# Optimization experiments

Hardware: AMD Instinct MI355X
Metric: run time of the kernel (lower is better)

The kernel has to match this reference:

```python
import jax, jax.numpy as jnp
import numpy as np
import math

B, C, H, W = 4, 256, 64, 64
E = 96  # embed_dim
SOFTMAX_SCALE = 10.0
RESIDUAL_SCALE_INIT = 0.1


def conv1x1(w, x):
    # w: [out_c, in_c], x: [b, in_c, h, w] -> [b, out_c, h, w]
    return jnp.einsum('oc,bchw->bohw', w, x)


def setup_inputs() -> dict:
    key = jax.random.key(0)
    ks = jax.random.split(key, 12)
    s = 0.02
    return {
        'x': jax.random.normal(ks[0], (B, C, H, W), jnp.float32),
        'mask': jax.random.uniform(ks[1], (B, 1, H, W), jnp.float32),
        'ln_gamma': jnp.ones((C,), jnp.float32),
        'ln_beta': jnp.zeros((C,), jnp.float32),
        'wq': jax.random.normal(ks[2], (E, C), jnp.float32) * s,
        'wk': jax.random.normal(ks[3], (E, C), jnp.float32) * s,
        'wv': jax.random.normal(ks[4], (C, C), jnp.float32) * s,
        'w_out': jax.random.normal(ks[5], (C, C), jnp.float32) * s,
        'w_qm': jax.random.normal(ks[6], (E, 1), jnp.float32) * s,
        'wd1': jax.random.normal(ks[7], (C, 2 * C), jnp.float32) * s,
        'wd2': jax.random.normal(ks[8], (C, C), jnp.float32) * s,
        'wg': jax.random.normal(ks[9], (C, C + 1), jnp.float32) * s,
        'residual_scale': jnp.asarray(RESIDUAL_SCALE_INIT, jnp.float32),
    }


def reference(x, mask, ln_gamma, ln_beta, wq, wk, wv, w_out, w_qm, wd1, wd2, wg,
              residual_scale):
    b, c, h, w = x.shape
    n = h * w

    # ChannelLayerNorm: LayerNorm over channel dim
    mu = jnp.mean(x, axis=1, keepdims=True)
    var = jnp.mean((x - mu) ** 2, axis=1, keepdims=True)
    x_norm = (x - mu) / jnp.sqrt(var + 1e-5)
    x_norm = x_norm * ln_gamma[None, :, None, None] + ln_beta[None, :, None, None]

    # Q/K/V projections (1x1 convs), flatten to [b, n, d]
    q = conv1x1(wq, x_norm) + conv1x1(w_qm, mask)
    q = q.reshape(b, E, n).transpose(0, 2, 1)        # [b, n, E]
    k = conv1x1(wk, x_norm).reshape(b, E, n).transpose(0, 2, 1)  # [b, n, E]
    v = conv1x1(wv, x).reshape(b, c, n).transpose(0, 2, 1)       # [b, n, C]

    # cosine normalization (F.normalize with eps=1e-12)
    q = q / jnp.clip(jnp.linalg.norm(q, axis=-1, keepdims=True), 1e-12)
    k = k / jnp.clip(jnp.linalg.norm(k, axis=-1, keepdims=True), 1e-12)

    scale = SOFTMAX_SCALE / math.sqrt(E)
    attn = jnp.einsum('bqe,bke->bqk', q, k) * scale  # [b, n, n]

    # keys with mask >= 0.5 are invalid -> bias -10000
    invalid_keys = (mask.reshape(b, 1, n) >= 0.5)    # [b, 1, n]
    attn = jnp.where(invalid_keys, jnp.float32(-10000.0), attn)
    attn = jax.nn.softmax(attn, axis=-1)

    attended = jnp.einsum('bqk,bkc->bqc', attn, v)   # [b, n, C]
    attended = attended.transpose(0, 2, 1).reshape(b, c, h, w)
    attended = conv1x1(w_out, attended)

    # delta correction branch
    corr_in = jnp.concatenate([attended - x, x_norm * mask], axis=1)  # [b, 2C, h, w]
    hidden = jax.nn.gelu(conv1x1(wd1, corr_in), approximate=False)
    corrective = conv1x1(wd2, hidden)

    # MaskConditionedGate (assumed): sigmoid(1x1 conv over [corrective, mask])
    gate_in = jnp.concatenate([corrective, mask], axis=1)  # [b, C+1, h, w]
    gate = jax.nn.sigmoid(conv1x1(wg, gate_in)) * mask

    delta = jnp.tanh(residual_scale) * gate * corrective
    return x + delta
```

## Files before the change

### kernel.cpp

```cpp
#include <hip/hip_runtime.h>
#include <hip/hip_bf16.h>
#include <math.h>

#define BB 4
#define CC 256
#define NN 4096
#define EE 96
#define NTOT (BB*NN)

typedef __attribute__((ext_vector_type(8))) short bf16x8;
typedef __attribute__((ext_vector_type(4))) float f32x4;

__device__ __forceinline__ short f2bf(float x) {
    __hip_bfloat16 h = __float2bfloat16(x);
    return *reinterpret_cast<short*>(&h);
}
__device__ __forceinline__ float bf2f(short s) {
    unsigned int u = ((unsigned int)(unsigned short)s) << 16;
    float f;
    __builtin_memcpy(&f, &u, 4);
    return f;
}
__device__ __forceinline__ float gelu_exact(float v) {
    return 0.5f * v * (1.0f + erff(v * 0.70710678118654752f));
}
__device__ __forceinline__ void gld16(void* lds, const void* g) {
    __builtin_amdgcn_global_load_lds(
        (const __attribute__((address_space(1))) unsigned int*)g,
        (__attribute__((address_space(3))) unsigned int*)lds, 16, 0, 0);
}

#define OFF_WQ  0
#define OFF_WK  24576
#define OFF_WV  49152
#define OFF_WO  114688
#define OFF_WD1 180224
#define OFF_WD2 311296
#define OFF_WG  376832
#define OFF_WGL 442368
#define W16_TOTAL 442624

__global__ void wconv_kernel(const float* __restrict__ wq, const float* __restrict__ wk,
                             const float* __restrict__ wv, const float* __restrict__ wo,
                             const float* __restrict__ wd1, const float* __restrict__ wd2,
                             const float* __restrict__ wg, short* __restrict__ W16) {
    int i = blockIdx.x * 256 + threadIdx.x;
    if (i >= W16_TOTAL) return;
    float v;
    if      (i < OFF_WK)  v = wq[i];
    else if (i < OFF_WV)  v = wk[i - OFF_WK];
    else if (i < OFF_WO)  v = wv[i - OFF_WV];
    else if (i < OFF_WD1) v = wo[i - OFF_WO];
    else if (i < OFF_WD2) v = wd1[i - OFF_WD1];
    else if (i < OFF_WG)  v = wd2[i - OFF_WD2];
    else if (i < OFF_WGL) { int l = i - OFF_WG; v = wg[(l >> 8) * 257 + (l & 255)]; }
    else                  v = wg[(i - OFF_WGL) * 257 + 256];
    W16[i] = f2bf(v);
}

__global__ __launch_bounds__(256) void lnproj_kernel(
    const float* __restrict__ x, const float* __restrict__ gamma,
    const float* __restrict__ beta, const short* __restrict__ W16,
    const float* __restrict__ mask, const float* __restrict__ w_qm,
    short* __restrict__ Xt16, short* __restrict__ Xn16,
    short* __restrict__ Q16, short* __restrict__ K16,
    short* __restrict__ V16t)
{
    __shared__ char ldsbuf[17408];
    float* tile = (float*)ldsbuf;
    short* Vt   = (short*)ldsbuf;
    __shared__ short Xn_lds[16 * 264];
    __shared__ short Xt_lds[16 * 264];
    __shared__ float psum[16][16], psq[16][16];
    __shared__ float mu_s[16], rs_s[16];
    __shared__ float gs[256], bs[256];

    const int tid = threadIdx.x;
    const int w = tid >> 6, lane = tid & 63, ln = lane & 15, quad = lane >> 4;
    const int b  = blockIdx.x >> 8;
    const int p0 = (blockIdx.x & 255) * 16;
    const int m0 = blockIdx.x * 16;
    const float* xb = x + (size_t)b * CC * NN;

    gs[tid] = gamma[tid];
    bs[tid] = beta[tid];
    #pragma unroll
    for (int i = 0; i < 4; ++i) {
        int idx = tid + i * 256;
        int c = idx >> 2, p4 = (idx & 3) * 4;
        float4 v = *(const float4*)&xb[(size_t)c * NN + p0 + p4];
        tile[c * 17 + p4]     = v.x;
        tile[c * 17 + p4 + 1] = v.y;
        tile[c * 17 + p4 + 2] = v.z;
        tile[c * 17 + p4 + 3] = v.w;
    }
    __syncthreads();
    {
        int col = tid & 15, part = tid >> 4;
        float s = 0.f, sq = 0.f;
        for (int r = part * 16; r < part * 16 + 16; ++r) {
            float v = tile[r * 17 + col];
            s += v; sq += v * v;
        }
        psum[part][col] = s; psq[part][col] = sq;
    }
    __syncthreads();
    if (tid < 16) {
        float S = 0.f, SQ = 0.f;
        #pragma unroll
        for (int j = 0; j < 16; ++j) { S += psum[j][tid]; SQ += psq[j][tid]; }
        float mu = S / 256.0f;
        float var = SQ / 256.0f - mu * mu;
        mu_s[tid] = mu;
        rs_s[tid] = rsqrtf(var + 1e-5f);
    }
    __syncthreads();
    #pragma unroll
    for (int i = 0; i < 2; ++i) {
        int idx = tid + i * 256;
        int p = idx >> 5, c8 = (idx & 31) * 8;
        float mu = mu_s[p], rcp = rs_s[p];
        bf16x8 xt, xn;
        #pragma unroll
        for (int j = 0; j < 8; ++j) {
            float v = tile[(c8 + j) * 17 + p];
            float n = (v - mu) * rcp * gs[c8 + j] + bs[c8 + j];
            xt[j] = f2bf(v); xn[j] = f2bf(n);
        }
        size_t o = (size_t)(m0 + p) * CC + c8;
        *(bf16x8*)&Xt16[o] = xt;
        *(bf16x8*)&Xn16[o] = xn;
        *(bf16x8*)&Xt_lds[p * 264 + c8] = xt;
        *(bf16x8*)&Xn_lds[p * 264 + c8] = xn;
    }
    asm volatile("s_waitcnt lgkmcnt(0)" ::: "memory");
    __builtin_amdgcn_s_barrier();
    __builtin_amdgcn_sched_barrier(0);

    if (w < 2) {
        const bool isQ = (w == 0);
        const int woff = isQ ? OFF_WQ : OFF_WK;

        f32x4 acc[6];
        #pragma unroll
        for (int i = 0; i < 6; ++i) acc[i] = (f32x4){0.f, 0.f, 0.f, 0.f};

        #pragma unroll
        for (int kt = 0; kt < 8; ++kt) {
            bf16x8 af = *(const bf16x8*)&Xn_lds[ln * 264 + kt * 32 + quad * 8];
            #pragma unroll
            for (int nt = 0; nt < 6; ++nt) {
                bf16x8 bf = *(const bf16x8*)&W16[woff + (size_t)(nt * 16 + ln) * 256 + kt * 32 + quad * 8];
                acc[nt] = __builtin_amdgcn_mfma_f32_16x16x32_bf16(af, bf, acc[nt], 0, 0, 0);
            }
        }

        short* outp = isQ ? Q16 : K16;
        #pragma unroll
        for (int r = 0; r < 4; ++r) {
            int row = m0 + quad * 4 + r;
            float mrow = isQ ? mask[row] : 0.f;
            float vals[6];
            float ss = 0.f;
            #pragma unroll
            for (int nt = 0; nt < 6; ++nt) {
                float v = acc[nt][r];
                if (isQ) v += mrow * w_qm[nt * 16 + ln];
                vals[nt] = v;
                ss += v * v;
            }
            ss += __shfl_xor(ss, 1, 64); ss += __shfl_xor(ss, 2, 64);
            ss += __shfl_xor(ss, 4, 64); ss += __shfl_xor(ss, 8, 64);
            float sc = 1.0f / fmaxf(sqrtf(ss), 1e-12f);
            #pragma unroll
            for (int nt = 0; nt < 6; ++nt)
                outp[(size_t)row * EE + nt * 16 + ln] = f2bf(vals[nt] * sc);
        }
    } else {
        const int wn = w - 2;

        f32x4 acc[8];
        #pragma unroll
        for (int i = 0; i < 8; ++i) acc[i] = (f32x4){0.f, 0.f, 0.f, 0.f};

        #pragma unroll
        for (int kt = 0; kt < 8; ++kt) {
            bf16x8 af = *(const bf16x8*)&Xt_lds[ln * 264 + kt * 32 + quad * 8];
            #pragma unroll
            for (int nt = 0; nt < 8; ++nt) {
                int col = wn * 128 + nt * 16 + ln;
                bf16x8 bf = *(const bf16x8*)&W16[OFF_WV + (size_t)col * 256 + kt * 32 + quad * 8];
                acc[nt] = __builtin_amdgcn_mfma_f32_16x16x32_bf16(af, bf, acc[nt], 0, 0, 0);
            }
        }
        #pragma unroll
        for (int nt = 0; nt < 8; ++nt) {
            int ch = wn * 128 + nt * 16 + ln;
            #pragma unroll
            for (int r = 0; r < 4; ++r)
                Vt[ch * 24 + quad * 4 + r] = f2bf(acc[nt][r]);
        }
    }
    asm volatile("s_waitcnt lgkmcnt(0)" ::: "memory");
    __builtin_amdgcn_s_barrier();
    __builtin_amdgcn_sched_barrier(0);

    #pragma unroll
    for (int i = 0; i < 2; ++i) {
        int idx = tid + i * 256;
        int ch = idx >> 1, p8 = (idx & 1) * 8;
        *(bf16x8*)&V16t[((size_t)b * CC + ch) * NN + p0 + p8] =
            *(const bf16x8*)&Vt[ch * 24 + p8];
    }
}

__global__ __launch_bounds__(256, 4) void attn_kernel(
    const short* __restrict__ Q16, const short* __restrict__ K16,
    const short* __restrict__ V16t, const float* __restrict__ mask,
    short* __restrict__ Opart, float* __restrict__ Lpart)
{
    __shared__ short Ks[2][3072];
    __shared__ short Ps[2][2560];

    const int tid = threadIdx.x;
    const int w = tid >> 6, lane = tid & 63, ln = lane & 15, quad = lane >> 4;
    const int bidx = blockIdx.x;
    const int kg = bidx >> 8;
    const int qg = bidx & 255;
    const int b  = (qg & 7) >> 1;
    const int qt = ((qg >> 3) << 1) | (qg & 1);
    const int q0 = qt * 64;
    const size_t bN = (size_t)b * NN;
    const size_t bCC = (size_t)b * CC;
    const int kbase = kg * 1024;
    const float C1 = 1.02062072615966f;
    const int wbase = w * 64;

    #define STAGEK(buf, kk)                                                         \
        do {                                                                        \
            gld16(&Ks[buf][wbase * 8],                                              \
                  &K16[(bN + (kk) + (tid & 31)) * EE + (tid >> 5) * 8]);            \
            if (w < 2)                                                              \
                gld16(&Ks[buf][(256 + wbase) * 8],                                  \
                      &K16[(bN + (kk) + (tid & 31)) * EE + (8 + (tid >> 5)) * 8]);  \
        } while (0)

    bf16x8 qf[3];
    #pragma unroll
    for (int e = 0; e < 3; ++e)
        qf[e] = *(const bf16x8*)&Q16[(bN + q0 + w * 16 + ln) * EE + e * 32 + quad * 8];

    f32x4 acc[4][4];
    #pragma unroll
    for (int mt = 0; mt < 4; ++mt)
        #pragma unroll
        for (int nt = 0; nt < 4; ++nt) acc[mt][nt] = (f32x4){0.f, 0.f, 0.f, 0.f};
    float lsum[4] = {0.f, 0.f, 0.f, 0.f};

    STAGEK(0, kbase);
    STAGEK(1, kbase + 32);
    __syncthreads();

    for (int it = 0; it < 32; ++it) {
        const int k0 = kbase + it * 32;
        const int cur = it & 1;

        bf16x8 vf[4];
        #pragma unroll
        for (int nt = 0; nt < 4; ++nt)
            vf[nt] = *(const bf16x8*)&V16t[(bCC + wbase + nt * 16 + ln) * NN + k0 + quad * 8];
        const float mk0 = mask[bN + k0 + ln];
        const float mk1 = mask[bN + k0 + 16 + ln];

        f32x4 s0 = (f32x4){0.f,0.f,0.f,0.f}, s1 = s0;
        __builtin_amdgcn_s_setprio(1);
        #pragma unroll
        for (int e = 0; e < 3; ++e) {
            bf16x8 kf0 = *(const bf16x8*)&Ks[cur][((e * 4 + quad) * 32 + ln) * 8];
            bf16x8 kf1 = *(const bf16x8*)&Ks[cur][((e * 4 + quad) * 32 + 16 + ln) * 8];
            s0 = __builtin_amdgcn_mfma_f32_16x16x32_bf16(qf[e], kf0, s0, 0, 0, 0);
            s1 = __builtin_amdgcn_mfma_f32_16x16x32_bf16(qf[e], kf1, s1, 0, 0, 0);
        }
        __builtin_amdgcn_s_setprio(0);
        const bool z0 = mk0 >= 0.5f;
        const bool z1 = mk1 >= 0.5f;
        #pragma unroll
        for (int r = 0; r < 4; ++r) {
            float p0 = z0 ? 0.f : __expf(fmaf(s0[r], C1, -C1));
            float p1 = z1 ? 0.f : __expf(fmaf(s1[r], C1, -C1));
            lsum[r] += p0 + p1;
            Ps[cur][(w * 16 + quad * 4 + r) * 40 + ln]      = f2bf(p0);
            Ps[cur][(w * 16 + quad * 4 + r) * 40 + 16 + ln] = f2bf(p1);
        }
        asm volatile("s_waitcnt vmcnt(0) lgkmcnt(0)" ::: "memory");
        __builtin_amdgcn_s_barrier();
        __builtin_amdgcn_sched_barrier(0);

        if (it + 2 < 32) STAGEK(cur, k0 + 64);

        __builtin_amdgcn_s_setprio(1);
        #pragma unroll
        for (int mt = 0; mt < 4; ++mt) {
            bf16x8 pf = *(const bf16x8*)&Ps[cur][(mt * 16 + ln) * 40 + quad * 8];
            #pragma unroll
            for (int nt = 0; nt < 4; ++nt)
                acc[mt][nt] = __builtin_amdgcn_mfma_f32_16x16x32_bf16(pf, vf[nt], acc[mt][nt], 0, 0, 0);
        }
        __builtin_amdgcn_s_setprio(0);
    }
    #undef STAGEK

    #pragma unroll
    for (int r = 0; r < 4; ++r) {
        float l = lsum[r];
        l += __shfl_xor(l, 1, 64); l += __shfl_xor(l, 2, 64);
        l += __shfl_xor(l, 4, 64); l += __shfl_xor(l, 8, 64);
        if (ln == 0)
            Lpart[(size_t)kg * NTOT + bN + q0 + w * 16 + quad * 4 + r] = l;
    }
    #pragma unroll
    for (int mt = 0; mt < 4; ++mt)
        #pragma unroll
        for (int nt = 0; nt < 4; ++nt)
            #pragma unroll
            for (int r = 0; r < 4; ++r)
                Opart[((size_t)kg * NTOT + bN + q0 + mt * 16 + quad * 4 + r) * 256
                      + wbase + nt * 16 + ln] = f2bf(acc[mt][nt][r]);
}

__global__ __launch_bounds__(256, 4) void epi_kernel(
    const short* __restrict__ Opart, const float* __restrict__ Lpart,
    const short* __restrict__ W16, const short* __restrict__ Xt16,
    const short* __restrict__ Xn16, const float* __restrict__ mask,
    const float* __restrict__ rs, const float* __restrict__ x,
    float* __restrict__ out)
{
    __shared__ char lds[37696];
    short* Olds  = (short*)lds;
    short* Clds  = (short*)lds;
    short* Dlds  = (short*)(lds + 8448);
    short* Hlds  = (short*)(lds + 25344);
    short* tileB = (short*)(lds + 25344);
    float* lsh   = (float*)(lds + 37632);

    const int tid = threadIdx.x;
    const int w = tid >> 6, lane = tid & 63, ln = lane & 15, quad = lane >> 4;
    const int m0 = blockIdx.x * 16;
    const int b = m0 >> 12, p0l = m0 & 4095;

    if (tid < 16) {
        int g = m0 + tid;
        lsh[tid] = 1.0f / (Lpart[g] + Lpart[NTOT + g] + Lpart[2 * NTOT + g] + Lpart[3 * NTOT + g]);
    }
    __syncthreads();

    #pragma unroll
    for (int i = 0; i < 2; ++i) {
        int idx = tid + i * 256;
        int q = idx >> 5, ch8 = (idx & 31) * 8;
        size_t base = (size_t)(m0 + q) * 256 + ch8;
        bf16x8 a0 = *(const bf16x8*)&Opart[base];
        bf16x8 a1 = *(const bf16x8*)&Opart[(size_t)NTOT * 256 + base];
        bf16x8 a2 = *(const bf16x8*)&Opart[(size_t)2 * NTOT * 256 + base];
        bf16x8 a3 = *(const bf16x8*)&Opart[(size_t)3 * NTOT * 256 + base];
        float linv = lsh[q];
        bf16x8 o;
        #pragma unroll
        for (int e = 0; e < 8; ++e)
            o[e] = f2bf((bf2f(a0[e]) + bf2f(a1[e]) + bf2f(a2[e]) + bf2f(a3[e])) * linv);
        *(bf16x8*)&Olds[q * 264 + ch8] = o;
        bf16x8 xn = *(const bf16x8*)&Xn16[base];
        float mq = mask[m0 + q];
        bf16x8 xm;
        #pragma unroll
        for (int e = 0; e < 8; ++e) xm[e] = f2bf(bf2f(xn[e]) * mq);
        *(bf16x8*)&Dlds[q * 528 + 256 + ch8] = xm;
    }
    __syncthreads();

    {
        f32x4 acc[4];
        #pragma unroll
        for (int i = 0; i < 4; ++i) acc[i] = (f32x4){0.f, 0.f, 0.f, 0.f};
        #pragma unroll
        for (int kt = 0; kt < 8; ++kt) {
            bf16x8 af = *(const bf16x8*)&Olds[ln * 264 + kt * 32 + quad * 8];
            #pragma unroll
            for (int nt = 0; nt < 4; ++nt) {
                int col = w * 64 + nt * 16 + ln;
                bf16x8 bf = *(const bf16x8*)&W16[OFF_WO + (size_t)col * 256 + kt * 32 + quad * 8];
                acc[nt] = __builtin_amdgcn_mfma_f32_16x16x32_bf16(af, bf, acc[nt], 0, 0, 0);
            }
        }
        #pragma unroll
        for (int nt = 0; nt < 4; ++nt) {
            int col = w * 64 + nt * 16 + ln;
            #pragma unroll
            for (int r = 0; r < 4; ++r) {
                int row = quad * 4 + r;
                float v = acc[nt][r] - bf2f(Xt16[(size_t)(m0 + row) * 256 + col]);
                Dlds[row * 528 + col] = f2bf(v);
            }
        }
    }
    __syncthreads();

    {
        f32x4 acc[4];
        #pragma unroll
        for (int i = 0; i < 4; ++i) acc[i] = (f32x4){0.f, 0.f, 0.f, 0.f};
        #pragma unroll
        for (int kt = 0; kt < 16; ++kt) {
            bf16x8 af = *(const bf16x8*)&Dlds[ln * 528 + kt * 32 + quad * 8];
            #pragma unroll
            for (int nt = 0; nt < 4; ++nt) {
                int col = w * 64 + nt * 16 + ln;
                bf16x8 bf = *(const bf16x8*)&W16[OFF_WD1 + (size_t)col * 512 + kt * 32 + quad * 8];
                acc[nt] = __builtin_amdgcn_mfma_f32_16x16x32_bf16(af, bf, acc[nt], 0, 0, 0);
            }
        }
        #pragma unroll
        for (int nt = 0; nt < 4; ++nt) {
            int col = w * 64 + nt * 16 + ln;
            #pragma unroll
            for (int r = 0; r < 4; ++r) {
                int row = quad * 4 + r;
                Hlds[row * 264 + col] = f2bf(gelu_exact(acc[nt][r]));
            }
        }
    }
    __syncthreads();

    {
        f32x4 acc[4];
        #pragma unroll
        for (int i = 0; i < 4; ++i) acc[i] = (f32x4){0.f, 0.f, 0.f, 0.f};
        #pragma unroll
        for (int kt = 0; kt < 8; ++kt) {
            bf16x8 af = *(const bf16x8*)&Hlds[ln * 264 + kt * 32 + quad * 8];
            #pragma unroll
            for (int nt = 0; nt < 4; ++nt) {
                int col = w * 64 + nt * 16 + ln;
                bf16x8 bf = *(const bf16x8*)&W16[OFF_WD2 + (size_t)col * 256 + kt * 32 + quad * 8];
                acc[nt] = __builtin_amdgcn_mfma_f32_16x16x32_bf16(af, bf, acc[nt], 0, 0, 0);
            }
        }
        #pragma unroll
        for (int nt = 0; nt < 4; ++nt) {
            int col = w * 64 + nt * 16 + ln;
            #pragma unroll
            for (int r = 0; r < 4; ++r) {
                int row = quad * 4 + r;
                Clds[row * 264 + col] = f2bf(acc[nt][r]);
            }
        }
    }
    __syncthreads();

    {
        f32x4 acc[4];
        #pragma unroll
        for (int i = 0; i < 4; ++i) acc[i] = (f32x4){0.f, 0.f, 0.f, 0.f};
        #pragma unroll
        for (int kt = 0; kt < 8; ++kt) {
            bf16x8 af = *(const bf16x8*)&Clds[ln * 264 + kt * 32 + quad * 8];
            #pragma unroll
            for (int nt = 0; nt < 4; ++nt) {
                int col = w * 64 + nt * 16 + ln;
                bf16x8 bf = *(const bf16x8*)&W16[OFF_WG + (size_t)col * 256 + kt * 32 + quad * 8];
                acc[nt] = __builtin_amdgcn_mfma_f32_16x16x32_bf16(af, bf, acc[nt], 0, 0, 0);
            }
        }
        float trs = tanhf(rs[0]);
        #pragma unroll
        for (int nt = 0; nt < 4; ++nt) {
            int col = w * 64 + nt * 16 + ln;
            float wgl = bf2f(W16[OFF_WGL + col]);
            #pragma unroll
            for (int r = 0; r < 4; ++r) {
                int row = quad * 4 + r;
                float mrow = mask[m0 + row];
                float logit = acc[nt][r] + mrow * wgl;
                float gate = mrow / (1.0f + __expf(-logit));
                float corr = bf2f(Clds[row * 264 + col]);
                tileB[col * 24 + row] = f2bf(trs * gate * corr);
            }
        }
    }
    __syncthreads();

    #pragma unroll
    for (int i = 0; i < 2; ++i) {
        int idx = tid + i * 256;
        int ch = idx >> 1, p8 = (idx & 1) * 8;
        bf16x8 d = *(const bf16x8*)&tileB[ch * 24 + p8];
        size_t o = ((size_t)b * CC + ch) * NN + p0l + p8;
        float4 x0 = *(const float4*)&x[o];
        float4 x1 = *(const float4*)&x[o + 4];
        float4 o0, o1;
        o0.x = x0.x + bf2f(d[0]); o0.y = x0.y + bf2f(d[1]);
        o0.z = x0.z + bf2f(d[2]); o0.w = x0.w + bf2f(d[3]);
        o1.x = x1.x + bf2f(d[4]); o1.y = x1.y + bf2f(d[5]);
        o1.z = x1.z + bf2f(d[6]); o1.w = x1.w + bf2f(d[7]);
        *(float4*)&out[o] = o0;
        *(float4*)&out[o + 4] = o1;
    }
}

extern "C" void kernel_launch(void* const* d_in, const int* in_sizes, int n_in,
                              void* d_out, int out_size, void* d_ws, size_t ws_size,
                              hipStream_t stream) {
    const float* x     = (const float*)d_in[0];
    const float* mask  = (const float*)d_in[1];
    const float* gamma = (const float*)d_in[2];
    const float* beta  = (const float*)d_in[3];
    const float* wq    = (const float*)d_in[4];
    const float* wk    = (const float*)d_in[5];
    const float* wv    = (const float*)d_in[6];
    const float* w_out = (const float*)d_in[7];
    const float* w_qm  = (const float*)d_in[8];
    const float* wd1   = (const float*)d_in[9];
    const float* wd2   = (const float*)d_in[10];
    const float* wg    = (const float*)d_in[11];
    const float* rs    = (const float*)d_in[12];
    float* out = (float*)d_out;

    const size_t NC = (size_t)NTOT * CC;
    const size_t NE = (size_t)NTOT * EE;
    short* Xn16  = (short*)d_ws;
    short* Xt16  = Xn16 + NC;
    short* Q16   = Xt16 + NC;
    short* K16   = Q16 + NE;
    short* V16t  = K16 + NE;
    short* W16   = V16t + NC;
    short* Opart = W16 + W16_TOTAL;
    float* Lpart = (float*)(Opart + 4 * NC);

    wconv_kernel<<<(W16_TOTAL + 255) / 256, 256, 0, stream>>>(wq, wk, wv, w_out,
                                                              wd1, wd2, wg, W16);
    lnproj_kernel<<<1024, 256, 0, stream>>>(x, gamma, beta, W16, mask, w_qm,
                                            Xt16, Xn16, Q16, K16, V16t);
    attn_kernel<<<1024, 256, 0, stream>>>(Q16, K16, V16t, mask, Opart, Lpart);
    epi_kernel<<<1024, 256, 0, stream>>>(Opart, Lpart, W16, Xt16, Xn16, mask,
                                         rs, x, out);
}
```

Measured before the change: 289.1 us.

## Hoist epilogue global loads, use exp2 softmax, bit-trick bf16 rounding, vectorize weight convert

Several independent micro-optimizations. A hand-written round-to-nearest-even bf16 conversion replaces the library call, and the softmax exponent is folded into exp2f with a prescaled constant. The weight-conversion kernel now handles four elements per thread with a vector store. The epilogue issues its Opart, Xn16, mask and Xt16 global loads before the first barrier so their latency overlaps the Lpart reduction, at the cost of more registers.

Result: no change. 293.9 us (+1.7%).

```diff
diff --git a/kernel.cpp b/kernel.cpp
--- a/kernel.cpp
+++ b/kernel.cpp
@@ -12,8 +12,10 @@
 typedef __attribute__((ext_vector_type(4))) float f32x4;
 
 __device__ __forceinline__ short f2bf(float x) {
-    __hip_bfloat16 h = __float2bfloat16(x);
-    return *reinterpret_cast<short*>(&h);
+    unsigned int u;
+    __builtin_memcpy(&u, &x, 4);
+    u += 0x7FFFu + ((u >> 16) & 1u);
+    return (short)(u >> 16);
 }
 __device__ __forceinline__ float bf2f(short s) {
     unsigned int u = ((unsigned int)(unsigned short)s) << 16;
@@ -44,18 +46,24 @@
                              const float* __restrict__ wv, const float* __restrict__ wo,
                              const float* __restrict__ wd1, const float* __restrict__ wd2,
                              const float* __restrict__ wg, short* __restrict__ W16) {
-    int i = blockIdx.x * 256 + threadIdx.x;
-    if (i >= W16_TOTAL) return;
-    float v;
-    if      (i < OFF_WK)  v = wq[i];
-    else if (i < OFF_WV)  v = wk[i - OFF_WK];
-    else if (i < OFF_WO)  v = wv[i - OFF_WV];
-    else if (i < OFF_WD1) v = wo[i - OFF_WO];
-    else if (i < OFF_WD2) v = wd1[i - OFF_WD1];
-    else if (i < OFF_WG)  v = wd2[i - OFF_WD2];
-    else if (i < OFF_WGL) { int l = i - OFF_WG; v = wg[(l >> 8) * 257 + (l & 255)]; }
-    else                  v = wg[(i - OFF_WGL) * 257 + 256];
-    W16[i] = f2bf(v);
+    int i0 = (blockIdx.x * 256 + threadIdx.x) * 4;
+    if (i0 >= W16_TOTAL) return;
+    short4 o;
+    #pragma unroll
+    for (int j = 0; j < 4; ++j) {
+        int i = i0 + j;
+        float v;
+        if      (i < OFF_WK)  v = wq[i];
+        else if (i < OFF_WV)  v = wk[i - OFF_WK];
+        else if (i < OFF_WO)  v = wv[i - OFF_WV];
+        else if (i < OFF_WD1) v = wo[i - OFF_WO];
+        else if (i < OFF_WD2) v = wd1[i - OFF_WD1];
+        else if (i < OFF_WG)  v = wd2[i - OFF_WD2];
+        else if (i < OFF_WGL) { int l = i - OFF_WG; v = wg[(l >> 8) * 257 + (l & 255)]; }
+        else                  v = wg[(i - OFF_WGL) * 257 + 256];
+        ((short*)&o)[j] = f2bf(v);
+    }
+    *(short4*)&W16[i0] = o;
 }
 
 __global__ __launch_bounds__(256) void lnproj_kernel(
@@ -233,7 +241,7 @@
     const size_t bN = (size_t)b * NN;
     const size_t bCC = (size_t)b * CC;
     const int kbase = kg * 1024;
-    const float C1 = 1.02062072615966f;
+    const float C2 = 1.47244446077890f;
     const int wbase = w * 64;
 
     #define STAGEK(buf, kk)                                                         \
@@ -286,8 +294,8 @@
         const bool z1 = mk1 >= 0.5f;
         #pragma unroll
         for (int r = 0; r < 4; ++r) {
-            float p0 = z0 ? 0.f : __expf(fmaf(s0[r], C1, -C1));
-            float p1 = z1 ? 0.f : __expf(fmaf(s1[r], C1, -C1));
+            float p0 = z0 ? 0.f : exp2f(fmaf(s0[r], C2, -C2));
+            float p1 = z1 ? 0.f : exp2f(fmaf(s1[r], C2, -C2));
             lsum[r] += p0 + p1;
             Ps[cur][(w * 16 + quad * 4 + r) * 40 + ln]      = f2bf(p0);
             Ps[cur][(w * 16 + quad * 4 + r) * 40 + 16 + ln] = f2bf(p1);
@@ -348,32 +356,46 @@
     const int m0 = blockIdx.x * 16;
     const int b = m0 >> 12, p0l = m0 & 4095;
 
-    if (tid < 16) {
-        int g = m0 + tid;
-        lsh[tid] = 1.0f / (Lpart[g] + Lpart[NTOT + g] + Lpart[2 * NTOT + g] + Lpart[3 * NTOT + g]);
-    }
-    __syncthreads();
-
+    bf16x8 ha0[2], ha1[2], ha2[2], ha3[2], hxn[2];
+    float  hmq[2];
     #pragma unroll
     for (int i = 0; i < 2; ++i) {
         int idx = tid + i * 256;
         int q = idx >> 5, ch8 = (idx & 31) * 8;
         size_t base = (size_t)(m0 + q) * 256 + ch8;
-        bf16x8 a0 = *(const bf16x8*)&Opart[base];
-        bf16x8 a1 = *(const bf16x8*)&Opart[(size_t)NTOT * 256 + base];
-        bf16x8 a2 = *(const bf16x8*)&Opart[(size_t)2 * NTOT * 256 + base];
-        bf16x8 a3 = *(const bf16x8*)&Opart[(size_t)3 * NTOT * 256 + base];
+        ha0[i] = *(const bf16x8*)&Opart[base];
+        ha1[i] = *(const bf16x8*)&Opart[(size_t)NTOT * 256 + base];
+        ha2[i] = *(const bf16x8*)&Opart[(size_t)2 * NTOT * 256 + base];
+        ha3[i] = *(const bf16x8*)&Opart[(size_t)3 * NTOT * 256 + base];
+        hxn[i] = *(const bf16x8*)&Xn16[base];
+        hmq[i] = mask[m0 + q];
+    }
+    short xtv[4][4];
+    #pragma unroll
+    for (int nt = 0; nt < 4; ++nt)
+        #pragma unroll
+        for (int r = 0; r < 4; ++r)
+            xtv[nt][r] = Xt16[(size_t)(m0 + quad * 4 + r) * 256 + (w * 64 + nt * 16 + ln)];
+
+    if (tid < 16) {
+        int g = m0 + tid;
+        lsh[tid] = 1.0f / (Lpart[g] + Lpart[NTOT + g] + Lpart[2 * NTOT + g] + Lpart[3 * NTOT + g]);
+    }
+    __syncthreads();
+
+    #pragma unroll
+    for (int i = 0; i < 2; ++i) {
+        int idx = tid + i * 256;
+        int q = idx >> 5, ch8 = (idx & 31) * 8;
         float linv = lsh[q];
         bf16x8 o;
         #pragma unroll
         for (int e = 0; e < 8; ++e)
-            o[e] = f2bf((bf2f(a0[e]) + bf2f(a1[e]) + bf2f(a2[e]) + bf2f(a3[e])) * linv);
+            o[e] = f2bf((bf2f(ha0[i][e]) + bf2f(ha1[i][e]) + bf2f(ha2[i][e]) + bf2f(ha3[i][e])) * linv);
         *(bf16x8*)&Olds[q * 264 + ch8] = o;
-        bf16x8 xn = *(const bf16x8*)&Xn16[base];
-        float mq = mask[m0 + q];
         bf16x8 xm;
         #pragma unroll
-        for (int e = 0; e < 8; ++e) xm[e] = f2bf(bf2f(xn[e]) * mq);
+        for (int e = 0; e < 8; ++e) xm[e] = f2bf(bf2f(hxn[i][e]) * hmq[i]);
         *(bf16x8*)&Dlds[q * 528 + 256 + ch8] = xm;
     }
     __syncthreads();
@@ -398,7 +420,7 @@
             #pragma unroll
             for (int r = 0; r < 4; ++r) {
                 int row = quad * 4 + r;
-                float v = acc[nt][r] - bf2f(Xt16[(size_t)(m0 + row) * 256 + col]);
+                float v = acc[nt][r] - bf2f(xtv[nt][r]);
                 Dlds[row * 528 + col] = f2bf(v);
             }
         }
@@ -536,8 +558,8 @@
     short* Opart = W16 + W16_TOTAL;
     float* Lpart = (float*)(Opart + 4 * NC);
 
-    wconv_kernel<<<(W16_TOTAL + 255) / 256, 256, 0, stream>>>(wq, wk, wv, w_out,
-                                                              wd1, wd2, wg, W16);
+    wconv_kernel<<<(W16_TOTAL / 4 + 255) / 256, 256, 0, stream>>>(wq, wk, wv, w_out,
+                                                                  wd1, wd2, wg, W16);
     lnproj_kernel<<<1024, 256, 0, stream>>>(x, gamma, beta, W16, mask, w_qm,
                                             Xt16, Xn16, Q16, K16, V16t);
     attn_kernel<<<1024, 256, 0, stream>>>(Q16, K16, V16t, mask, Opart, Lpart);
```
